# Kernel optimization log

Hardware: AMD Instinct MI355X
Metric: run time of the kernel (lower is better)

## Reference

```python
import jax, jax.numpy as jnp
import numpy as np

MARGIN = 0.5  # hardcoded in the torch __init__ regardless of the margin arg
P_IDS, K_PER_ID, K_PER_MOD = 32, 8, 4
B, C = P_IDS * K_PER_ID, 1024


def setup_inputs() -> dict:
    key = jax.random.key(0)
    inputs = jax.random.normal(key, (B, C), dtype=jnp.float32)
    # Standard cross-modal ReID sampler: P identities, K instances each,
    # first K/2 from modality 0, last K/2 from modality 1. This guarantees the
    # boolean-mask reshape in the original code is well-formed (M per row).
    targets = jnp.repeat(jnp.arange(P_IDS, dtype=jnp.int32), K_PER_ID)
    subs = jnp.tile(jnp.repeat(jnp.arange(2, dtype=jnp.int32), K_PER_MOD), P_IDS)
    return {"inputs": inputs, "targets": targets, "subs": subs, "m_count": K_PER_MOD}


def _loss(inputs, targets, subs, m_count):
    b, c = inputs.shape
    # Mask construction uses detached inputs in the original (clone().detach()).
    xs = jax.lax.stop_gradient(inputs)
    diff = jnp.abs(xs[:, None, :] - xs[None, :, :])                     # (B,B,C)
    identity_mask = targets[:, None] == targets[None, :]                # (B,B)
    modality_mask = subs[:, None] == subs[None, :]                      # (B,B)
    combined = identity_mask & modality_mask                            # (B,B)

    # diff[combined].reshape(B, M, C): every row has exactly m_count trues;
    # stable argsort recovers the selected column indices in ascending order,
    # matching torch's row-major boolean-mask gather.
    order = jnp.argsort(jnp.where(combined, 0, 1), axis=1)              # stable
    idx = order[:, :m_count]                                            # (B,M)
    modality_diff = jnp.take_along_axis(diff, idx[:, :, None], axis=1)  # (B,M,C)

    mean_md = modality_diff.mean(-1, keepdims=True)                     # (B,M,1)
    m_counts = (modality_diff < mean_md * MARGIN).sum(1)                # (B,C) int
    # mdm[i,j,c] = m_counts[i,c] * m_counts[j,c]  (detached float mask)
    mdm = (m_counts[:, None, :] * m_counts[None, :, :]).astype(inputs.dtype)  # (B,B,C)

    mean_d = diff.mean(-1, keepdims=True)                               # (B,B,1)
    idm = (diff < mean_d * MARGIN).astype(inputs.dtype)                 # (B,B,C)

    # Gradient-carrying pairwise differences (vectorized form of the B-loop).
    d = inputs[:, None, :] - inputs[None, :, :]                         # (B,B,C)
    mod_dist = jnp.sqrt(jnp.maximum(((d * mdm) ** 2).sum(-1), 1e-12))   # (B,B)
    id_dist = jnp.sqrt(jnp.maximum(((d * idm) ** 2).sum(-1), 1e-12))    # (B,B)
    id_dist = jnp.where(identity_mask, jnp.inf, id_dist)                # drop same-id

    per_row = jnp.maximum(mod_dist.max(axis=1) * 10.0 - id_dist.min(axis=1), 0.0)
    return per_row.mean()


def reference(inputs, targets, subs, m_count):
    return _loss(inputs, targets, subs, m_count)
```

## Files before the change

### kernel.cpp

```cpp
#include <hip/hip_runtime.h>
#include <math.h>

#define BB 256
#define CC 1024
#define CC4 (CC/4)
#define MARGIN 0.5f
#define NSL 8
#define LDST 132


__global__ __launch_bounds__(64) void mcsq_kernel(
    const float* __restrict__ x, const int* __restrict__ targets,
    const int* __restrict__ subs, const int* __restrict__ m_count_p,
    float* __restrict__ mcsq, float* __restrict__ acc,
    unsigned int* __restrict__ cnt_g)
{
    const int i = blockIdx.x;
    const int lane = threadIdx.x;
    if (i == 0 && lane == 0) { *acc = 0.f; *cnt_g = 0u; }
    const int ti = targets[i], si = subs[i];
    int mc = *m_count_p;
    if (mc > 8) mc = 8;

    unsigned long long masks[4];
    #pragma unroll
    for (int q = 0; q < 4; ++q) {
        const int j = q * 64 + lane;
        masks[q] = __ballot(targets[j] == ti && subs[j] == si);
    }
    int idx[8];
    int cnt = 0;
    for (int q = 0; q < 4 && cnt < mc; ++q) {
        unsigned long long m = masks[q];
        while (m && cnt < mc) {
            const int b = __ffsll(m) - 1;
            idx[cnt++] = q * 64 + b;
            m &= m - 1;
        }
    }
    for (int q = 0; q < 4 && cnt < mc; ++q) {
        unsigned long long m = ~masks[q];
        while (m && cnt < mc) {
            const int b = __ffsll(m) - 1;
            idx[cnt++] = q * 64 + b;
            m &= m - 1;
        }
    }

    const float4* x4 = (const float4*)x;
    float4 xi[4];
    #pragma unroll
    for (int t = 0; t < 4; ++t) xi[t] = x4[(long)i * CC4 + lane + 64 * t];

    float4 c4[4];
    #pragma unroll
    for (int t = 0; t < 4; ++t) c4[t] = make_float4(0.f, 0.f, 0.f, 0.f);

    for (int k = 0; k < cnt; ++k) {
        float4 ad[4];
        float s = 0.f;
        #pragma unroll
        for (int t = 0; t < 4; ++t) {
            const float4 xj = x4[(long)idx[k] * CC4 + lane + 64 * t];
            ad[t].x = fabsf(xi[t].x - xj.x);
            ad[t].y = fabsf(xi[t].y - xj.y);
            ad[t].z = fabsf(xi[t].z - xj.z);
            ad[t].w = fabsf(xi[t].w - xj.w);
            s += ad[t].x + ad[t].y + ad[t].z + ad[t].w;
        }
        #pragma unroll
        for (int off = 32; off > 0; off >>= 1) s += __shfl_xor(s, off, 64);
        const float thr = s * (MARGIN / CC);
        #pragma unroll
        for (int t = 0; t < 4; ++t) {
            c4[t].x += (ad[t].x < thr) ? 1.f : 0.f;
            c4[t].y += (ad[t].y < thr) ? 1.f : 0.f;
            c4[t].z += (ad[t].z < thr) ? 1.f : 0.f;
            c4[t].w += (ad[t].w < thr) ? 1.f : 0.f;
        }
    }
    float4* m4 = (float4*)mcsq;
    #pragma unroll
    for (int t = 0; t < 4; ++t) {
        float4 o;
        o.x = c4[t].x * c4[t].x;
        o.y = c4[t].y * c4[t].y;
        o.z = c4[t].z * c4[t].z;
        o.w = c4[t].w * c4[t].w;
        m4[(long)i * CC4 + lane + 64 * t] = o;
    }
}

__global__ __launch_bounds__(256) void pass1_kernel(
    const float* __restrict__ x, float* __restrict__ S_part)
{
    __shared__ float xs[64 * LDST];
    const int b  = blockIdx.x;
    const int cc = b & 7;
    const int jt = (b >> 3) & 7;
    const int it = b >> 6;
    const int l  = threadIdx.x;

    const float4* x4 = (const float4*)x;
    #pragma unroll
    for (int k = 0; k < 8; ++k) {
        const int idx = l + 256 * k;
        const int row = idx >> 5;
        const int c4  = idx & 31;
        const int grow = (row < 32) ? (it * 32 + row) : (jt * 32 + row - 32);
        *(float4*)&xs[row * LDST + c4 * 4] = x4[grow * CC4 + cc * 32 + c4];
    }
    __syncthreads();

    const int li = l >> 4, lj = l & 15;
    const float4* pi0 = (const float4*)&xs[(2 * li) * LDST];
    const float4* pi1 = (const float4*)&xs[(2 * li + 1) * LDST];
    const float4* pj0 = (const float4*)&xs[(32 + 2 * lj) * LDST];
    const float4* pj1 = (const float4*)&xs[(32 + 2 * lj + 1) * LDST];
    float s00 = 0.f, s01 = 0.f, s10 = 0.f, s11 = 0.f;
    #pragma unroll 8
    for (int q = 0; q < 32; ++q) {
        const float4 a0 = pi0[q], a1 = pi1[q], b0 = pj0[q], b1 = pj1[q];
        s00 += fabsf(a0.x - b0.x) + fabsf(a0.y - b0.y) + fabsf(a0.z - b0.z) + fabsf(a0.w - b0.w);
        s01 += fabsf(a0.x - b1.x) + fabsf(a0.y - b1.y) + fabsf(a0.z - b1.z) + fabsf(a0.w - b1.w);
        s10 += fabsf(a1.x - b0.x) + fabsf(a1.y - b0.y) + fabsf(a1.z - b0.z) + fabsf(a1.w - b0.w);
        s11 += fabsf(a1.x - b1.x) + fabsf(a1.y - b1.y) + fabsf(a1.z - b1.z) + fabsf(a1.w - b1.w);
    }
    const int gi0 = it * 32 + 2 * li, gj0 = jt * 32 + 2 * lj;
    float* Sp = S_part + cc * (BB * BB);
    Sp[gi0 * BB + gj0]           = s00;
    Sp[gi0 * BB + gj0 + 1]       = s01;
    Sp[(gi0 + 1) * BB + gj0]     = s10;
    Sp[(gi0 + 1) * BB + gj0 + 1] = s11;
}

__global__ __launch_bounds__(256) void thr_kernel(
    const float* __restrict__ S_part, float* __restrict__ THR)
{
    const int g = blockIdx.x * 256 + threadIdx.x;
    float s = 0.f;
    #pragma unroll
    for (int cc = 0; cc < NSL; ++cc) s += S_part[cc * (BB * BB) + g];
    THR[g] = s * (MARGIN / CC);
}

__global__ __launch_bounds__(256) void pass2_kernel(
    const float* __restrict__ x, const float* __restrict__ mcsq,
    const float* __restrict__ THR,
    float* __restrict__ IDS_part, float* __restrict__ MD_part)
{
    __shared__ float xs[64 * LDST];
    __shared__ float ms[64 * LDST];
    const int b  = blockIdx.x;
    const int cc = b & 7;
    const int jt = (b >> 3) & 7;
    const int it = b >> 6;
    const int l  = threadIdx.x;

    const float4* x4 = (const float4*)x;
    const float4* m4 = (const float4*)mcsq;
    #pragma unroll
    for (int k = 0; k < 8; ++k) {
        const int idx = l + 256 * k;
        const int row = idx >> 5;
        const int c4  = idx & 31;
        const int grow = (row < 32) ? (it * 32 + row) : (jt * 32 + row - 32);
        *(float4*)&xs[row * LDST + c4 * 4] = x4[grow * CC4 + cc * 32 + c4];
        *(float4*)&ms[row * LDST + c4 * 4] = m4[grow * CC4 + cc * 32 + c4];
    }
    const int li = l >> 4, lj = l & 15;
    const int gi0 = it * 32 + 2 * li, gj0 = jt * 32 + 2 * lj;
    const float t00 = THR[gi0 * BB + gj0];
    const float t01 = THR[gi0 * BB + gj0 + 1];
    const float t10 = THR[(gi0 + 1) * BB + gj0];
    const float t11 = THR[(gi0 + 1) * BB + gj0 + 1];
    __syncthreads();

    const float4* pi0 = (const float4*)&xs[(2 * li) * LDST];
    const float4* pi1 = (const float4*)&xs[(2 * li + 1) * LDST];
    const float4* pj0 = (const float4*)&xs[(32 + 2 * lj) * LDST];
    const float4* pj1 = (const float4*)&xs[(32 + 2 * lj + 1) * LDST];
    const float4* qi0 = (const float4*)&ms[(2 * li) * LDST];
    const float4* qi1 = (const float4*)&ms[(2 * li + 1) * LDST];
    const float4* qj0 = (const float4*)&ms[(32 + 2 * lj) * LDST];
    const float4* qj1 = (const float4*)&ms[(32 + 2 * lj + 1) * LDST];

    float i00 = 0.f, i01 = 0.f, i10 = 0.f, i11 = 0.f;
    float m00 = 0.f, m01 = 0.f, m10 = 0.f, m11 = 0.f;
    #pragma unroll 4
    for (int q = 0; q < 32; ++q) {
        const float4 a0 = pi0[q], a1 = pi1[q], b0 = pj0[q], b1 = pj1[q];
        const float4 wa0 = qi0[q], wa1 = qi1[q], wb0 = qj0[q], wb1 = qj1[q];
        #pragma unroll
        for (int u = 0; u < 4; ++u) {
            const float xa0 = (&a0.x)[u], xa1 = (&a1.x)[u];
            const float xb0 = (&b0.x)[u], xb1 = (&b1.x)[u];
            const float va0 = (&wa0.x)[u], va1 = (&wa1.x)[u];
            const float vb0 = (&wb0.x)[u], vb1 = (&wb1.x)[u];
            float d, qq;
            d = xa0 - xb0; qq = d * d; i00 += (fabsf(d) < t00) ? qq : 0.f; m00 += qq * va0 * vb0;
            d = xa0 - xb1; qq = d * d; i01 += (fabsf(d) < t01) ? qq : 0.f; m01 += qq * va0 * vb1;
            d = xa1 - xb0; qq = d * d; i10 += (fabsf(d) < t10) ? qq : 0.f; m10 += qq * va1 * vb0;
            d = xa1 - xb1; qq = d * d; i11 += (fabsf(d) < t11) ? qq : 0.f; m11 += qq * va1 * vb1;
        }
    }
    float* Ip = IDS_part + cc * (BB * BB);
    float* Mp = MD_part  + cc * (BB * BB);
    Ip[gi0 * BB + gj0]           = i00;
    Ip[gi0 * BB + gj0 + 1]       = i01;
    Ip[(gi0 + 1) * BB + gj0]     = i10;
    Ip[(gi0 + 1) * BB + gj0 + 1] = i11;
    Mp[gi0 * BB + gj0]           = m00;
    Mp[gi0 * BB + gj0 + 1]       = m01;
    Mp[(gi0 + 1) * BB + gj0]     = m10;
    Mp[(gi0 + 1) * BB + gj0 + 1] = m11;
}

__global__ __launch_bounds__(64) void final_kernel(
    const float* __restrict__ IDS_part, const float* __restrict__ MD_part,
    const int* __restrict__ targets,
    float* __restrict__ acc, unsigned int* __restrict__ cnt_g,
    float* __restrict__ out)
{
    const int i = blockIdx.x;
    const int lane = threadIdx.x;
    const int ti = targets[i];

    float4 idv = make_float4(0.f, 0.f, 0.f, 0.f);
    float4 mdv = make_float4(0.f, 0.f, 0.f, 0.f);
    #pragma unroll
    for (int cc = 0; cc < NSL; ++cc) {
        const float4 a = ((const float4*)(IDS_part + cc * (BB * BB) + i * BB))[lane];
        const float4 b = ((const float4*)(MD_part  + cc * (BB * BB) + i * BB))[lane];
        idv.x += a.x; idv.y += a.y; idv.z += a.z; idv.w += a.w;
        mdv.x += b.x; mdv.y += b.y; mdv.z += b.z; mdv.w += b.w;
    }
    const int4 tjv = ((const int4*)targets)[lane];

    float mx, mn;
    mx =           sqrtf(fmaxf(mdv.x, 1e-12f));
    mx = fmaxf(mx, sqrtf(fmaxf(mdv.y, 1e-12f)));
    mx = fmaxf(mx, sqrtf(fmaxf(mdv.z, 1e-12f)));
    mx = fmaxf(mx, sqrtf(fmaxf(mdv.w, 1e-12f)));
    mn =           (tjv.x != ti) ? sqrtf(fmaxf(idv.x, 1e-12f)) : INFINITY;
    mn = fminf(mn, (tjv.y != ti) ? sqrtf(fmaxf(idv.y, 1e-12f)) : INFINITY);
    mn = fminf(mn, (tjv.z != ti) ? sqrtf(fmaxf(idv.z, 1e-12f)) : INFINITY);
    mn = fminf(mn, (tjv.w != ti) ? sqrtf(fmaxf(idv.w, 1e-12f)) : INFINITY);

    #pragma unroll
    for (int off = 32; off > 0; off >>= 1) {
        mx = fmaxf(mx, __shfl_xor(mx, off, 64));
        mn = fminf(mn, __shfl_xor(mn, off, 64));
    }
    if (lane == 0) {
        const float per = fmaxf(mx * 10.f - mn, 0.f);
        atomicAdd(acc, per * (1.0f / BB));
        __threadfence();
        const unsigned int old = atomicAdd(cnt_g, 1u);
        if (old == BB - 1) {
            __threadfence();
            out[0] = atomicAdd(acc, 0.0f);
        }
    }
}

extern "C" void kernel_launch(void* const* d_in, const int* in_sizes, int n_in,
                              void* d_out, int out_size, void* d_ws, size_t ws_size,
                              hipStream_t stream)
{
    const float* x       = (const float*)d_in[0];
    const int*   targets = (const int*)d_in[1];
    const int*   subs    = (const int*)d_in[2];
    const int*   m_count = (const int*)d_in[3];
    float* out  = (float*)d_out;

    float* mcsq     = (float*)d_ws;
    float* S_part   = mcsq     + (long)BB * CC;
    float* THR      = S_part   + NSL * BB * BB;
    float* IDS_part = THR      + BB * BB;
    float* MD_part  = IDS_part + NSL * BB * BB;
    float* acc      = MD_part  + NSL * BB * BB;
    unsigned int* cnt_g = (unsigned int*)(acc + 1);

    mcsq_kernel <<<BB,  64,  0, stream>>>(x, targets, subs, m_count, mcsq, acc, cnt_g);
    pass1_kernel<<<512, 256, 0, stream>>>(x, S_part);
    thr_kernel  <<<256, 256, 0, stream>>>(S_part, THR);
    pass2_kernel<<<512, 256, 0, stream>>>(x, mcsq, THR, IDS_part, MD_part);
    final_kernel<<<BB,  64,  0, stream>>>(IDS_part, MD_part, targets, acc, cnt_g, out);
}
```

Baseline: 99.33 us.

## Fuse all loss stages into one cooperative kernel with grid-wide syncs

Replaces the five-kernel chain (mcsq, pass1, thr, pass2, final) with a single cooperative mega-kernel of 512 blocks that uses grid.sync between phases. The mcsq work is folded into the last 64 blocks after the L1-sum pass, and the threshold reduction is done inline per block instead of through a separate thr kernel and THR buffer. The aim is to remove launch gaps and intermediate kernel boundaries. In exchange it depends on cooperative launch residency (two blocks per CU) and grid-sync cost, with the old path kept as a fallback.

Result: slower. 201.0 us (+102.4%).

```diff
diff --git a/kernel.cpp b/kernel.cpp
--- a/kernel.cpp
+++ b/kernel.cpp
@@ -1,13 +1,260 @@
 #include <hip/hip_runtime.h>
+#include <hip/hip_cooperative_groups.h>
 #include <math.h>
+
+namespace cg = cooperative_groups;
 
 #define BB 256
 #define CC 1024
 #define CC4 (CC/4)
 #define MARGIN 0.5f
 #define NSL 8
+#define LDSM 68
 #define LDST 132
 
+
+__global__ __launch_bounds__(256, 2) void mega_kernel(
+    const float* __restrict__ x, const int* __restrict__ targets,
+    const int* __restrict__ subs, const int* __restrict__ m_count_p,
+    float* __restrict__ mcsq, float* __restrict__ S_part,
+    float* __restrict__ IDS_part, float* __restrict__ MD_part,
+    float* __restrict__ acc, unsigned int* __restrict__ cnt_g,
+    float* __restrict__ out)
+{
+    cg::grid_group grid = cg::this_grid();
+    __shared__ float xs[64 * LDSM];
+    __shared__ float ms[64 * LDSM];
+    const int b = blockIdx.x;
+    const int l = threadIdx.x;
+    const int cc = b & 7, jt = (b >> 3) & 7, it = b >> 6;
+    const float4* x4 = (const float4*)x;
+    const int li = l >> 4, lj = l & 15;
+    const int gi0 = it * 32 + 2 * li, gj0 = jt * 32 + 2 * lj;
+
+    if (b == 0 && l == 0) { *acc = 0.f; *cnt_g = 0u; }
+
+    #pragma unroll
+    for (int k = 0; k < 4; ++k) {
+        const int idx = l + 256 * k;
+        const int row = idx >> 4;
+        const int c4  = idx & 15;
+        const int grow = (row < 32) ? (it * 32 + row) : (jt * 32 + row - 32);
+        *(float4*)&xs[row * LDSM + c4 * 4] = x4[grow * CC4 + cc * 32 + c4];
+        *(float4*)&ms[row * LDSM + c4 * 4] = x4[grow * CC4 + cc * 32 + 16 + c4];
+    }
+    __syncthreads();
+    {
+        float s00 = 0.f, s01 = 0.f, s10 = 0.f, s11 = 0.f;
+        #pragma unroll
+        for (int h = 0; h < 2; ++h) {
+            const float* buf = h ? ms : xs;
+            const float4* pi0 = (const float4*)&buf[(2 * li) * LDSM];
+            const float4* pi1 = (const float4*)&buf[(2 * li + 1) * LDSM];
+            const float4* pj0 = (const float4*)&buf[(32 + 2 * lj) * LDSM];
+            const float4* pj1 = (const float4*)&buf[(32 + 2 * lj + 1) * LDSM];
+            #pragma unroll 8
+            for (int q = 0; q < 16; ++q) {
+                const float4 a0 = pi0[q], a1 = pi1[q], b0 = pj0[q], b1 = pj1[q];
+                s00 += fabsf(a0.x - b0.x) + fabsf(a0.y - b0.y) + fabsf(a0.z - b0.z) + fabsf(a0.w - b0.w);
+                s01 += fabsf(a0.x - b1.x) + fabsf(a0.y - b1.y) + fabsf(a0.z - b1.z) + fabsf(a0.w - b1.w);
+                s10 += fabsf(a1.x - b0.x) + fabsf(a1.y - b0.y) + fabsf(a1.z - b0.z) + fabsf(a1.w - b0.w);
+                s11 += fabsf(a1.x - b1.x) + fabsf(a1.y - b1.y) + fabsf(a1.z - b1.z) + fabsf(a1.w - b1.w);
+            }
+        }
+        float* Sp = S_part + cc * (BB * BB);
+        Sp[gi0 * BB + gj0]           = s00;
+        Sp[gi0 * BB + gj0 + 1]       = s01;
+        Sp[(gi0 + 1) * BB + gj0]     = s10;
+        Sp[(gi0 + 1) * BB + gj0 + 1] = s11;
+    }
+
+    if (b >= 448) {
+        const int lane = l & 63;
+        const int i = (b - 448) * 4 + (l >> 6);
+        const int ti = targets[i], si = subs[i];
+        int mc = *m_count_p;
+        if (mc > 8) mc = 8;
+
+        unsigned long long masks[4];
+        #pragma unroll
+        for (int q = 0; q < 4; ++q) {
+            const int j = q * 64 + lane;
+            masks[q] = __ballot(targets[j] == ti && subs[j] == si);
+        }
+        int idx[8];
+        int cnt = 0;
+        for (int q = 0; q < 4 && cnt < mc; ++q) {
+            unsigned long long m = masks[q];
+            while (m && cnt < mc) {
+                const int bb2 = __ffsll(m) - 1;
+                idx[cnt++] = q * 64 + bb2;
+                m &= m - 1;
+            }
+        }
+        for (int q = 0; q < 4 && cnt < mc; ++q) {
+            unsigned long long m = ~masks[q];
+            while (m && cnt < mc) {
+                const int bb2 = __ffsll(m) - 1;
+                idx[cnt++] = q * 64 + bb2;
+                m &= m - 1;
+            }
+        }
+
+        float4 xi[4];
+        #pragma unroll
+        for (int t = 0; t < 4; ++t) xi[t] = x4[(long)i * CC4 + lane + 64 * t];
+        float4 c4v[4];
+        #pragma unroll
+        for (int t = 0; t < 4; ++t) c4v[t] = make_float4(0.f, 0.f, 0.f, 0.f);
+
+        for (int k = 0; k < cnt; ++k) {
+            float4 ad[4];
+            float s = 0.f;
+            #pragma unroll
+            for (int t = 0; t < 4; ++t) {
+                const float4 xj = x4[(long)idx[k] * CC4 + lane + 64 * t];
+                ad[t].x = fabsf(xi[t].x - xj.x);
+                ad[t].y = fabsf(xi[t].y - xj.y);
+                ad[t].z = fabsf(xi[t].z - xj.z);
+                ad[t].w = fabsf(xi[t].w - xj.w);
+                s += ad[t].x + ad[t].y + ad[t].z + ad[t].w;
+            }
+            #pragma unroll
+            for (int off = 32; off > 0; off >>= 1) s += __shfl_xor(s, off, 64);
+            const float thr = s * (MARGIN / CC);
+            #pragma unroll
+            for (int t = 0; t < 4; ++t) {
+                c4v[t].x += (ad[t].x < thr) ? 1.f : 0.f;
+                c4v[t].y += (ad[t].y < thr) ? 1.f : 0.f;
+                c4v[t].z += (ad[t].z < thr) ? 1.f : 0.f;
+                c4v[t].w += (ad[t].w < thr) ? 1.f : 0.f;
+            }
+        }
+        float4* mout = (float4*)mcsq;
+        #pragma unroll
+        for (int t = 0; t < 4; ++t) {
+            float4 o;
+            o.x = c4v[t].x * c4v[t].x;
+            o.y = c4v[t].y * c4v[t].y;
+            o.z = c4v[t].z * c4v[t].z;
+            o.w = c4v[t].w * c4v[t].w;
+            mout[(long)i * CC4 + lane + 64 * t] = o;
+        }
+    }
+
+    grid.sync();
+
+    {
+        float t00 = 0.f, t01 = 0.f, t10 = 0.f, t11 = 0.f;
+        #pragma unroll
+        for (int s = 0; s < NSL; ++s) {
+            const float* Sp = S_part + s * (BB * BB);
+            t00 += Sp[gi0 * BB + gj0];
+            t01 += Sp[gi0 * BB + gj0 + 1];
+            t10 += Sp[(gi0 + 1) * BB + gj0];
+            t11 += Sp[(gi0 + 1) * BB + gj0 + 1];
+        }
+        t00 *= (MARGIN / CC); t01 *= (MARGIN / CC);
+        t10 *= (MARGIN / CC); t11 *= (MARGIN / CC);
+
+        const float4* m4 = (const float4*)mcsq;
+        float i00 = 0.f, i01 = 0.f, i10 = 0.f, i11 = 0.f;
+        float m00 = 0.f, m01 = 0.f, m10 = 0.f, m11 = 0.f;
+        for (int h = 0; h < 2; ++h) {
+            __syncthreads();
+            #pragma unroll
+            for (int k = 0; k < 4; ++k) {
+                const int idx = l + 256 * k;
+                const int row = idx >> 4;
+                const int c4  = idx & 15;
+                const int grow = (row < 32) ? (it * 32 + row) : (jt * 32 + row - 32);
+                *(float4*)&xs[row * LDSM + c4 * 4] = x4[grow * CC4 + cc * 32 + h * 16 + c4];
+                *(float4*)&ms[row * LDSM + c4 * 4] = m4[grow * CC4 + cc * 32 + h * 16 + c4];
+            }
+            __syncthreads();
+            const float4* pi0 = (const float4*)&xs[(2 * li) * LDSM];
+            const float4* pi1 = (const float4*)&xs[(2 * li + 1) * LDSM];
+            const float4* pj0 = (const float4*)&xs[(32 + 2 * lj) * LDSM];
+            const float4* pj1 = (const float4*)&xs[(32 + 2 * lj + 1) * LDSM];
+            const float4* qi0 = (const float4*)&ms[(2 * li) * LDSM];
+            const float4* qi1 = (const float4*)&ms[(2 * li + 1) * LDSM];
+            const float4* qj0 = (const float4*)&ms[(32 + 2 * lj) * LDSM];
+            const float4* qj1 = (const float4*)&ms[(32 + 2 * lj + 1) * LDSM];
+            #pragma unroll 4
+            for (int q = 0; q < 16; ++q) {
+                const float4 a0 = pi0[q], a1 = pi1[q], b0 = pj0[q], b1 = pj1[q];
+                const float4 wa0 = qi0[q], wa1 = qi1[q], wb0 = qj0[q], wb1 = qj1[q];
+                #pragma unroll
+                for (int u = 0; u < 4; ++u) {
+                    const float xa0 = (&a0.x)[u], xa1 = (&a1.x)[u];
+                    const float xb0 = (&b0.x)[u], xb1 = (&b1.x)[u];
+                    const float va0 = (&wa0.x)[u], va1 = (&wa1.x)[u];
+                    const float vb0 = (&wb0.x)[u], vb1 = (&wb1.x)[u];
+                    float d, qq;
+                    d = xa0 - xb0; qq = d * d; i00 += (fabsf(d) < t00) ? qq : 0.f; m00 += qq * va0 * vb0;
+                    d = xa0 - xb1; qq = d * d; i01 += (fabsf(d) < t01) ? qq : 0.f; m01 += qq * va0 * vb1;
+                    d = xa1 - xb0; qq = d * d; i10 += (fabsf(d) < t10) ? qq : 0.f; m10 += qq * va1 * vb0;
+                    d = xa1 - xb1; qq = d * d; i11 += (fabsf(d) < t11) ? qq : 0.f; m11 += qq * va1 * vb1;
+                }
+            }
+        }
+        float* Ip = IDS_part + cc * (BB * BB);
+        float* Mp = MD_part  + cc * (BB * BB);
+        Ip[gi0 * BB + gj0]           = i00;
+        Ip[gi0 * BB + gj0 + 1]       = i01;
+        Ip[(gi0 + 1) * BB + gj0]     = i10;
+        Ip[(gi0 + 1) * BB + gj0 + 1] = i11;
+        Mp[gi0 * BB + gj0]           = m00;
+        Mp[gi0 * BB + gj0 + 1]       = m01;
+        Mp[(gi0 + 1) * BB + gj0]     = m10;
+        Mp[(gi0 + 1) * BB + gj0 + 1] = m11;
+    }
+
+    grid.sync();
+
+    if (b < 64) {
+        const int lane = l & 63;
+        const int i = b * 4 + (l >> 6);
+        const int ti = targets[i];
+
+        float4 idv = make_float4(0.f, 0.f, 0.f, 0.f);
+        float4 mdv = make_float4(0.f, 0.f, 0.f, 0.f);
+        #pragma unroll
+        for (int s = 0; s < NSL; ++s) {
+            const float4 a = ((const float4*)(IDS_part + s * (BB * BB) + i * BB))[lane];
+            const float4 c = ((const float4*)(MD_part  + s * (BB * BB) + i * BB))[lane];
+            idv.x += a.x; idv.y += a.y; idv.z += a.z; idv.w += a.w;
+            mdv.x += c.x; mdv.y += c.y; mdv.z += c.z; mdv.w += c.w;
+        }
+        const int4 tjv = ((const int4*)targets)[lane];
+
+        float mx, mn;
+        mx =           sqrtf(fmaxf(mdv.x, 1e-12f));
+        mx = fmaxf(mx, sqrtf(fmaxf(mdv.y, 1e-12f)));
+        mx = fmaxf(mx, sqrtf(fmaxf(mdv.z, 1e-12f)));
+        mx = fmaxf(mx, sqrtf(fmaxf(mdv.w, 1e-12f)));
+        mn =           (tjv.x != ti) ? sqrtf(fmaxf(idv.x, 1e-12f)) : INFINITY;
+        mn = fminf(mn, (tjv.y != ti) ? sqrtf(fmaxf(idv.y, 1e-12f)) : INFINITY);
+        mn = fminf(mn, (tjv.z != ti) ? sqrtf(fmaxf(idv.z, 1e-12f)) : INFINITY);
+        mn = fminf(mn, (tjv.w != ti) ? sqrtf(fmaxf(idv.w, 1e-12f)) : INFINITY);
+
+        #pragma unroll
+        for (int off = 32; off > 0; off >>= 1) {
+            mx = fmaxf(mx, __shfl_xor(mx, off, 64));
+            mn = fminf(mn, __shfl_xor(mn, off, 64));
+        }
+        if (lane == 0) {
+            const float per = fmaxf(mx * 10.f - mn, 0.f);
+            atomicAdd(acc, per * (1.0f / BB));
+            __threadfence();
+            const unsigned int old = atomicAdd(cnt_g, 1u);
+            if (old == BB - 1) {
+                __threadfence();
+                out[0] = atomicAdd(acc, 0.0f);
+            }
+        }
+    }
+}
 
 __global__ __launch_bounds__(64) void mcsq_kernel(
     const float* __restrict__ x, const int* __restrict__ targets,
@@ -51,7 +298,6 @@
     float4 xi[4];
     #pragma unroll
     for (int t = 0; t < 4; ++t) xi[t] = x4[(long)i * CC4 + lane + 64 * t];
-
     float4 c4[4];
     #pragma unroll
     for (int t = 0; t < 4; ++t) c4[t] = make_float4(0.f, 0.f, 0.f, 0.f);
@@ -282,9 +528,22 @@
     float* acc      = MD_part  + NSL * BB * BB;
     unsigned int* cnt_g = (unsigned int*)(acc + 1);
 
-    mcsq_kernel <<<BB,  64,  0, stream>>>(x, targets, subs, m_count, mcsq, acc, cnt_g);
-    pass1_kernel<<<512, 256, 0, stream>>>(x, S_part);
-    thr_kernel  <<<256, 256, 0, stream>>>(S_part, THR);
-    pass2_kernel<<<512, 256, 0, stream>>>(x, mcsq, THR, IDS_part, MD_part);
-    final_kernel<<<BB,  64,  0, stream>>>(IDS_part, MD_part, targets, acc, cnt_g, out);
-}
+    bool coop_ok = false;
+    int maxB = 0;
+    if (hipOccupancyMaxActiveBlocksPerMultiprocessor(&maxB, mega_kernel, 256, 0)
+            == hipSuccess && maxB >= 2) {
+        void* args[] = {(void*)&x, (void*)&targets, (void*)&subs, (void*)&m_count,
+                        (void*)&mcsq, (void*)&S_part, (void*)&IDS_part, (void*)&MD_part,
+                        (void*)&acc, (void*)&cnt_g, (void*)&out};
+        if (hipLaunchCooperativeKernel((const void*)mega_kernel, dim3(512),
+                                       dim3(256), args, 0, stream) == hipSuccess)
+            coop_ok = true;
+    }
+    if (!coop_ok) {
+        mcsq_kernel <<<BB,  64,  0, stream>>>(x, targets, subs, m_count, mcsq, acc, cnt_g);
+        pass1_kernel<<<512, 256, 0, stream>>>(x, S_part);
+        thr_kernel  <<<256, 256, 0, stream>>>(S_part, THR);
+        pass2_kernel<<<512, 256, 0, stream>>>(x, mcsq, THR, IDS_part, MD_part);
+        final_kernel<<<BB,  64,  0, stream>>>(IDS_part, MD_part, targets, acc, cnt_g, out);
+    }
+}
```

## Fuse mcsq into pass1, fold threshold reduction into pass2, split channels finer

Applied to the files above, without the earlier changes.

Five launches become three. The modality-count work now runs in the tail blocks of pass1, and pass2 sums the eight S_part slices itself instead of relying on a separate threshold kernel. pass2 now splits channels into 16 slices instead of 8, which doubles its block count and halves its shared memory per block. The aim is less launch overhead and more parallelism and occupancy in pass2, at the cost of twice as many partial-sum slices for final_kernel to read and redundant S_part reads across pass2 blocks.

After: 98.37 us. About the same (-1.0%).

```diff
diff --git a/kernel.cpp b/kernel.cpp
--- a/kernel.cpp
+++ b/kernel.cpp
@@ -5,94 +5,17 @@
 #define CC 1024
 #define CC4 (CC/4)
 #define MARGIN 0.5f
-#define NSL 8
+#define NSL1 8
+#define NSL2 16
 #define LDST 132
-
-
-__global__ __launch_bounds__(64) void mcsq_kernel(
+#define LDSM 68
+
+
+__global__ __launch_bounds__(256) void pass1_kernel(
     const float* __restrict__ x, const int* __restrict__ targets,
     const int* __restrict__ subs, const int* __restrict__ m_count_p,
-    float* __restrict__ mcsq, float* __restrict__ acc,
-    unsigned int* __restrict__ cnt_g)
-{
-    const int i = blockIdx.x;
-    const int lane = threadIdx.x;
-    if (i == 0 && lane == 0) { *acc = 0.f; *cnt_g = 0u; }
-    const int ti = targets[i], si = subs[i];
-    int mc = *m_count_p;
-    if (mc > 8) mc = 8;
-
-    unsigned long long masks[4];
-    #pragma unroll
-    for (int q = 0; q < 4; ++q) {
-        const int j = q * 64 + lane;
-        masks[q] = __ballot(targets[j] == ti && subs[j] == si);
-    }
-    int idx[8];
-    int cnt = 0;
-    for (int q = 0; q < 4 && cnt < mc; ++q) {
-        unsigned long long m = masks[q];
-        while (m && cnt < mc) {
-            const int b = __ffsll(m) - 1;
-            idx[cnt++] = q * 64 + b;
-            m &= m - 1;
-        }
-    }
-    for (int q = 0; q < 4 && cnt < mc; ++q) {
-        unsigned long long m = ~masks[q];
-        while (m && cnt < mc) {
-            const int b = __ffsll(m) - 1;
-            idx[cnt++] = q * 64 + b;
-            m &= m - 1;
-        }
-    }
-
-    const float4* x4 = (const float4*)x;
-    float4 xi[4];
-    #pragma unroll
-    for (int t = 0; t < 4; ++t) xi[t] = x4[(long)i * CC4 + lane + 64 * t];
-
-    float4 c4[4];
-    #pragma unroll
-    for (int t = 0; t < 4; ++t) c4[t] = make_float4(0.f, 0.f, 0.f, 0.f);
-
-    for (int k = 0; k < cnt; ++k) {
-        float4 ad[4];
-        float s = 0.f;
-        #pragma unroll
-        for (int t = 0; t < 4; ++t) {
-            const float4 xj = x4[(long)idx[k] * CC4 + lane + 64 * t];
-            ad[t].x = fabsf(xi[t].x - xj.x);
-            ad[t].y = fabsf(xi[t].y - xj.y);
-            ad[t].z = fabsf(xi[t].z - xj.z);
-            ad[t].w = fabsf(xi[t].w - xj.w);
-            s += ad[t].x + ad[t].y + ad[t].z + ad[t].w;
-        }
-        #pragma unroll
-        for (int off = 32; off > 0; off >>= 1) s += __shfl_xor(s, off, 64);
-        const float thr = s * (MARGIN / CC);
-        #pragma unroll
-        for (int t = 0; t < 4; ++t) {
-            c4[t].x += (ad[t].x < thr) ? 1.f : 0.f;
-            c4[t].y += (ad[t].y < thr) ? 1.f : 0.f;
-            c4[t].z += (ad[t].z < thr) ? 1.f : 0.f;
-            c4[t].w += (ad[t].w < thr) ? 1.f : 0.f;
-        }
-    }
-    float4* m4 = (float4*)mcsq;
-    #pragma unroll
-    for (int t = 0; t < 4; ++t) {
-        float4 o;
-        o.x = c4[t].x * c4[t].x;
-        o.y = c4[t].y * c4[t].y;
-        o.z = c4[t].z * c4[t].z;
-        o.w = c4[t].w * c4[t].w;
-        m4[(long)i * CC4 + lane + 64 * t] = o;
-    }
-}
-
-__global__ __launch_bounds__(256) void pass1_kernel(
-    const float* __restrict__ x, float* __restrict__ S_part)
+    float* __restrict__ mcsq, float* __restrict__ S_part,
+    float* __restrict__ acc, unsigned int* __restrict__ cnt_g)
 {
     __shared__ float xs[64 * LDST];
     const int b  = blockIdx.x;
@@ -100,6 +23,7 @@
     const int jt = (b >> 3) & 7;
     const int it = b >> 6;
     const int l  = threadIdx.x;
+    if (b == 0 && l == 0) { *acc = 0.f; *cnt_g = 0u; }
 
     const float4* x4 = (const float4*)x;
     #pragma unroll
@@ -132,63 +56,135 @@
     Sp[gi0 * BB + gj0 + 1]       = s01;
     Sp[(gi0 + 1) * BB + gj0]     = s10;
     Sp[(gi0 + 1) * BB + gj0 + 1] = s11;
-}
-
-__global__ __launch_bounds__(256) void thr_kernel(
-    const float* __restrict__ S_part, float* __restrict__ THR)
-{
-    const int g = blockIdx.x * 256 + threadIdx.x;
-    float s = 0.f;
-    #pragma unroll
-    for (int cc = 0; cc < NSL; ++cc) s += S_part[cc * (BB * BB) + g];
-    THR[g] = s * (MARGIN / CC);
+
+    if (b >= 448) {
+        const int lane = l & 63;
+        const int i = (b - 448) * 4 + (l >> 6);
+        const int ti = targets[i], si = subs[i];
+        int mc = *m_count_p;
+        if (mc > 8) mc = 8;
+
+        unsigned long long masks[4];
+        #pragma unroll
+        for (int q = 0; q < 4; ++q) {
+            const int j = q * 64 + lane;
+            masks[q] = __ballot(targets[j] == ti && subs[j] == si);
+        }
+        int idx[8];
+        int cnt = 0;
+        for (int q = 0; q < 4 && cnt < mc; ++q) {
+            unsigned long long m = masks[q];
+            while (m && cnt < mc) {
+                const int bb2 = __ffsll(m) - 1;
+                idx[cnt++] = q * 64 + bb2;
+                m &= m - 1;
+            }
+        }
+        for (int q = 0; q < 4 && cnt < mc; ++q) {
+            unsigned long long m = ~masks[q];
+            while (m && cnt < mc) {
+                const int bb2 = __ffsll(m) - 1;
+                idx[cnt++] = q * 64 + bb2;
+                m &= m - 1;
+            }
+        }
+
+        float4 xi[4];
+        #pragma unroll
+        for (int t = 0; t < 4; ++t) xi[t] = x4[(long)i * CC4 + lane + 64 * t];
+        float4 c4v[4];
+        #pragma unroll
+        for (int t = 0; t < 4; ++t) c4v[t] = make_float4(0.f, 0.f, 0.f, 0.f);
+
+        for (int k = 0; k < cnt; ++k) {
+            float4 ad[4];
+            float s = 0.f;
+            #pragma unroll
+            for (int t = 0; t < 4; ++t) {
+                const float4 xj = x4[(long)idx[k] * CC4 + lane + 64 * t];
+                ad[t].x = fabsf(xi[t].x - xj.x);
+                ad[t].y = fabsf(xi[t].y - xj.y);
+                ad[t].z = fabsf(xi[t].z - xj.z);
+                ad[t].w = fabsf(xi[t].w - xj.w);
+                s += ad[t].x + ad[t].y + ad[t].z + ad[t].w;
+            }
+            #pragma unroll
+            for (int off = 32; off > 0; off >>= 1) s += __shfl_xor(s, off, 64);
+            const float thr = s * (MARGIN / CC);
+            #pragma unroll
+            for (int t = 0; t < 4; ++t) {
+                c4v[t].x += (ad[t].x < thr) ? 1.f : 0.f;
+                c4v[t].y += (ad[t].y < thr) ? 1.f : 0.f;
+                c4v[t].z += (ad[t].z < thr) ? 1.f : 0.f;
+                c4v[t].w += (ad[t].w < thr) ? 1.f : 0.f;
+            }
+        }
+        float4* mout = (float4*)mcsq;
+        #pragma unroll
+        for (int t = 0; t < 4; ++t) {
+            float4 o;
+            o.x = c4v[t].x * c4v[t].x;
+            o.y = c4v[t].y * c4v[t].y;
+            o.z = c4v[t].z * c4v[t].z;
+            o.w = c4v[t].w * c4v[t].w;
+            mout[(long)i * CC4 + lane + 64 * t] = o;
+        }
+    }
 }
 
 __global__ __launch_bounds__(256) void pass2_kernel(
     const float* __restrict__ x, const float* __restrict__ mcsq,
-    const float* __restrict__ THR,
+    const float* __restrict__ S_part,
     float* __restrict__ IDS_part, float* __restrict__ MD_part)
 {
-    __shared__ float xs[64 * LDST];
-    __shared__ float ms[64 * LDST];
+    __shared__ float xs[64 * LDSM];
+    __shared__ float ms[64 * LDSM];
     const int b  = blockIdx.x;
-    const int cc = b & 7;
-    const int jt = (b >> 3) & 7;
-    const int it = b >> 6;
+    const int cc = b & 15;
+    const int jt = (b >> 4) & 7;
+    const int it = b >> 7;
     const int l  = threadIdx.x;
 
     const float4* x4 = (const float4*)x;
     const float4* m4 = (const float4*)mcsq;
     #pragma unroll
-    for (int k = 0; k < 8; ++k) {
+    for (int k = 0; k < 4; ++k) {
         const int idx = l + 256 * k;
-        const int row = idx >> 5;
-        const int c4  = idx & 31;
+        const int row = idx >> 4;
+        const int c4  = idx & 15;
         const int grow = (row < 32) ? (it * 32 + row) : (jt * 32 + row - 32);
-        *(float4*)&xs[row * LDST + c4 * 4] = x4[grow * CC4 + cc * 32 + c4];
-        *(float4*)&ms[row * LDST + c4 * 4] = m4[grow * CC4 + cc * 32 + c4];
-    }
+        *(float4*)&xs[row * LDSM + c4 * 4] = x4[grow * CC4 + cc * 16 + c4];
+        *(float4*)&ms[row * LDSM + c4 * 4] = m4[grow * CC4 + cc * 16 + c4];
+    }
+
     const int li = l >> 4, lj = l & 15;
     const int gi0 = it * 32 + 2 * li, gj0 = jt * 32 + 2 * lj;
-    const float t00 = THR[gi0 * BB + gj0];
-    const float t01 = THR[gi0 * BB + gj0 + 1];
-    const float t10 = THR[(gi0 + 1) * BB + gj0];
-    const float t11 = THR[(gi0 + 1) * BB + gj0 + 1];
+    float t00 = 0.f, t01 = 0.f, t10 = 0.f, t11 = 0.f;
+    #pragma unroll
+    for (int s = 0; s < NSL1; ++s) {
+        const float* Sp = S_part + s * (BB * BB);
+        t00 += Sp[gi0 * BB + gj0];
+        t01 += Sp[gi0 * BB + gj0 + 1];
+        t10 += Sp[(gi0 + 1) * BB + gj0];
+        t11 += Sp[(gi0 + 1) * BB + gj0 + 1];
+    }
+    t00 *= (MARGIN / CC); t01 *= (MARGIN / CC);
+    t10 *= (MARGIN / CC); t11 *= (MARGIN / CC);
     __syncthreads();
 
-    const float4* pi0 = (const float4*)&xs[(2 * li) * LDST];
-    const float4* pi1 = (const float4*)&xs[(2 * li + 1) * LDST];
-    const float4* pj0 = (const float4*)&xs[(32 + 2 * lj) * LDST];
-    const float4* pj1 = (const float4*)&xs[(32 + 2 * lj + 1) * LDST];
-    const float4* qi0 = (const float4*)&ms[(2 * li) * LDST];
-    const float4* qi1 = (const float4*)&ms[(2 * li + 1) * LDST];
-    const float4* qj0 = (const float4*)&ms[(32 + 2 * lj) * LDST];
-    const float4* qj1 = (const float4*)&ms[(32 + 2 * lj + 1) * LDST];
+    const float4* pi0 = (const float4*)&xs[(2 * li) * LDSM];
+    const float4* pi1 = (const float4*)&xs[(2 * li + 1) * LDSM];
+    const float4* pj0 = (const float4*)&xs[(32 + 2 * lj) * LDSM];
+    const float4* pj1 = (const float4*)&xs[(32 + 2 * lj + 1) * LDSM];
+    const float4* qi0 = (const float4*)&ms[(2 * li) * LDSM];
+    const float4* qi1 = (const float4*)&ms[(2 * li + 1) * LDSM];
+    const float4* qj0 = (const float4*)&ms[(32 + 2 * lj) * LDSM];
+    const float4* qj1 = (const float4*)&ms[(32 + 2 * lj + 1) * LDSM];
 
     float i00 = 0.f, i01 = 0.f, i10 = 0.f, i11 = 0.f;
     float m00 = 0.f, m01 = 0.f, m10 = 0.f, m11 = 0.f;
     #pragma unroll 4
-    for (int q = 0; q < 32; ++q) {
+    for (int q = 0; q < 16; ++q) {
         const float4 a0 = pi0[q], a1 = pi1[q], b0 = pj0[q], b1 = pj1[q];
         const float4 wa0 = qi0[q], wa1 = qi1[q], wb0 = qj0[q], wb1 = qj1[q];
         #pragma unroll
@@ -229,11 +225,11 @@
     float4 idv = make_float4(0.f, 0.f, 0.f, 0.f);
     float4 mdv = make_float4(0.f, 0.f, 0.f, 0.f);
     #pragma unroll
-    for (int cc = 0; cc < NSL; ++cc) {
+    for (int cc = 0; cc < NSL2; ++cc) {
         const float4 a = ((const float4*)(IDS_part + cc * (BB * BB) + i * BB))[lane];
-        const float4 b = ((const float4*)(MD_part  + cc * (BB * BB) + i * BB))[lane];
+        const float4 c = ((const float4*)(MD_part  + cc * (BB * BB) + i * BB))[lane];
         idv.x += a.x; idv.y += a.y; idv.z += a.z; idv.w += a.w;
-        mdv.x += b.x; mdv.y += b.y; mdv.z += b.z; mdv.w += b.w;
+        mdv.x += c.x; mdv.y += c.y; mdv.z += c.z; mdv.w += c.w;
     }
     const int4 tjv = ((const int4*)targets)[lane];
 
@@ -276,15 +272,14 @@
 
     float* mcsq     = (float*)d_ws;
     float* S_part   = mcsq     + (long)BB * CC;
-    float* THR      = S_part   + NSL * BB * BB;
-    float* IDS_part = THR      + BB * BB;
-    float* MD_part  = IDS_part + NSL * BB * BB;
-    float* acc      = MD_part  + NSL * BB * BB;
+    float* IDS_part = S_part   + NSL1 * BB * BB;
+    float* MD_part  = IDS_part + NSL2 * BB * BB;
+    float* acc      = MD_part  + NSL2 * BB * BB;
     unsigned int* cnt_g = (unsigned int*)(acc + 1);
 
-    mcsq_kernel <<<BB,  64,  0, stream>>>(x, targets, subs, m_count, mcsq, acc, cnt_g);
-    pass1_kernel<<<512, 256, 0, stream>>>(x, S_part);
-    thr_kernel  <<<256, 256, 0, stream>>>(S_part, THR);
-    pass2_kernel<<<512, 256, 0, stream>>>(x, mcsq, THR, IDS_part, MD_part);
-    final_kernel<<<BB,  64,  0, stream>>>(IDS_part, MD_part, targets, acc, cnt_g, out);
-}
+    pass1_kernel<<<512,  256, 0, stream>>>(x, targets, subs, m_count, mcsq,
+                                           S_part, acc, cnt_g);
+    pass2_kernel<<<1024, 256, 0, stream>>>(x, mcsq, S_part, IDS_part, MD_part);
+    final_kernel<<<BB,   64,  0, stream>>>(IDS_part, MD_part, targets,
+                                           acc, cnt_g, out);
+}
```
